# Optimization experiments

Measured on AMD Instinct MI355X. Metric: run time of the kernel, lower is better.

Reference implementation:

```python
import jax, jax.numpy as jnp
import numpy as np

DIM = 128
NUM_LAYERS = 5
EPS = 1e-5


def setup_inputs() -> dict:
    key = jax.random.key(0)
    ks = jax.random.split(key, 16)
    N, E, D = 50000, 640000, DIM
    x = jax.random.uniform(ks[0], (N, 3), dtype=jnp.float32)
    edge_index = jax.random.randint(ks[1], (2, E), 0, N, dtype=jnp.int64)
    norm = jax.random.uniform(ks[2], (E,), dtype=jnp.float32)
    s3 = 1.0 / np.sqrt(3.0)
    sd = 1.0 / np.sqrt(D)
    return {
        "x": x,
        "edge_index": edge_index,
        "norm": norm,
        "W_enc": jax.random.uniform(ks[3], (D, 3), jnp.float32, -s3, s3),
        "bn_e_gamma": jnp.ones((D,), jnp.float32),
        "bn_e_beta": jnp.zeros((D,), jnp.float32),
        "W_ih": jax.random.uniform(ks[4], (3 * D, D), jnp.float32, -sd, sd),
        "W_hh": jax.random.uniform(ks[5], (3 * D, D), jnp.float32, -sd, sd),
        "b_ih": jax.random.uniform(ks[6], (3 * D,), jnp.float32, -sd, sd),
        "b_hh": jax.random.uniform(ks[7], (3 * D,), jnp.float32, -sd, sd),
        "W_dec": jax.random.uniform(ks[8], (D // 2, D), jnp.float32, -sd, sd),
        "bn_d_gamma": jnp.ones((D // 2,), jnp.float32),
        "bn_d_beta": jnp.zeros((D // 2,), jnp.float32),
        "W_dec2": jax.random.uniform(ks[9], (1, D // 2), jnp.float32, -sd * np.sqrt(2.0), sd * np.sqrt(2.0)),
    }


def batchnorm(h, gamma, beta):
    # training-mode BatchNorm1d: biased batch stats over the node dimension
    mu = jnp.mean(h, axis=0)
    var = jnp.var(h, axis=0)
    return (h - mu) * jax.lax.rsqrt(var + EPS) * gamma + beta


def gru_cell(inp, hid, W_ih, W_hh, b_ih, b_hh):
    gi = inp @ W_ih.T + b_ih  # [N, 3D]
    gh = hid @ W_hh.T + b_hh
    D = hid.shape[1]
    i_r, i_z, i_n = gi[:, :D], gi[:, D:2 * D], gi[:, 2 * D:]
    h_r, h_z, h_n = gh[:, :D], gh[:, D:2 * D], gh[:, 2 * D:]
    r = jax.nn.sigmoid(i_r + h_r)
    z = jax.nn.sigmoid(i_z + h_z)
    n = jnp.tanh(i_n + r * h_n)
    return (1.0 - z) * n + z * hid


def reference(x, edge_index, norm, W_enc, bn_e_gamma, bn_e_beta, W_ih, W_hh, b_ih, b_hh, W_dec, bn_d_gamma, bn_d_beta, W_dec2):
    N = x.shape[0]
    src, dst = edge_index[0], edge_index[1]
    # encode
    h = jax.nn.relu(batchnorm(x @ W_enc.T, bn_e_gamma, bn_e_beta))  # [N, D]
    h_sum = h
    prev_h = h
    for _ in range(NUM_LAYERS):
        # neighborhood aggregation: scatter-add of norm-weighted source features
        msg = norm[:, None] * prev_h[src]  # [E, D]
        h_agg = jax.ops.segment_sum(msg, dst, num_segments=N)  # [N, D]
        h_sum = h_sum + h_agg
        prev_h = gru_cell(h_agg, prev_h, W_ih, W_hh, b_ih, b_hh)
    z = h_sum / (NUM_LAYERS + 1)  # mean over stacked h_list
    # decode
    y = jax.nn.relu(batchnorm(z @ W_dec.T, bn_d_gamma, bn_d_beta))
    y = y @ W_dec2.T  # [N, 1]
    return y.reshape(-1)
```

## Files before the change

kernel.cpp:

```cpp
#include <hip/hip_runtime.h>

#define DD 128

typedef _Float16 f16x8 __attribute__((ext_vector_type(8)));
typedef unsigned short u16x8 __attribute__((ext_vector_type(8)));
typedef float f32x4 __attribute__((ext_vector_type(4)));

__device__ __forceinline__ float sigmoidf_(float v){ return 1.f/(1.f+__expf(-v)); }
__device__ __forceinline__ float tanhf_(float v){
  float e2 = __expf(2.f*v);
  return 1.f - 2.f/(e2 + 1.f);
}
__device__ __forceinline__ float h2f(unsigned short u){
  _Float16 h; __builtin_memcpy(&h, &u, 2); return (float)h;
}
__device__ __forceinline__ unsigned short f2h(float v){
  _Float16 h = (_Float16)v; unsigned short u; __builtin_memcpy(&u, &h, 2); return u;
}

#define PREP_B 416
__global__ void __launch_bounds__(256) k_pre1(
        const float* __restrict__ W_ih, const float* __restrict__ W_hh,
        const float* __restrict__ W_dec, const float* __restrict__ x,
        const float* __restrict__ W_enc, const int* __restrict__ dst,
        unsigned short* __restrict__ Wih_h, unsigned short* __restrict__ Whh_h,
        unsigned short* __restrict__ Wd_h, float* __restrict__ h0, float* __restrict__ stats,
        int* __restrict__ counts, int N, int E){
  const int tid = threadIdx.x;
  const int gb = blockIdx.x;
  const int TOT = 384*128;
  if (gb < PREP_B){
    int idx = gb*256 + tid;
    if (idx < 2*TOT){
      const float* W = (idx < TOT) ? W_ih : W_hh;
      unsigned short* D = (idx < TOT) ? Wih_h : Whh_h;
      int fi = (idx < TOT) ? idx : idx - TOT;
      int t = fi & 7;
      int l = (fi >> 3) & 63;
      int ks = (fi >> 9) & 3;
      int nt = fi >> 11;
      int fg = nt / 3, gate = nt % 3;
      int j = gate*128 + fg*16 + (l & 15);
      int k = ks*32 + ((l >> 4) & 3)*8 + t;
      D[fi] = f2h(W[j*128 + k]);
    } else if (idx < 2*TOT + 64*128){
      int fi2 = idx - 2*TOT;
      int t  = fi2 & 7;
      int l  = (fi2 >> 3) & 63;
      int ks = (fi2 >> 9) & 3;
      int jt = fi2 >> 11;
      int j = jt*16 + (l & 15);
      int k = ks*32 + ((l >> 4) & 3)*8 + t;
      Wd_h[fi2] = f2h(W_dec[j*128 + k]);
    }
  } else if (gb < PREP_B + 256){
    const int b = gb - PREP_B;
    const int f = tid & 127;
    const int sub = tid >> 7;
    const float w0 = W_enc[f*3], w1 = W_enc[f*3+1], w2 = W_enc[f*3+2];
    const int chunk = (N + 255) / 256;
    const int n0 = b * chunk;
    const int n1 = (n0 + chunk < N) ? (n0 + chunk) : N;
    float s = 0.f, q = 0.f;
    for (int n = n0 + sub; n < n1; n += 2){
      float x0 = x[n*3], x1 = x[n*3+1], x2 = x[n*3+2];
      float h = x0*w0 + x1*w1 + x2*w2;
      h0[(size_t)n*DD + f] = h;
      s += h; q += h*h;
    }
    atomicAdd(&stats[f], s);
    atomicAdd(&stats[DD+f], q);
  } else {
    int e = (gb - PREP_B - 256)*256 + tid;
    if (e < E) atomicAdd(&counts[dst[e]], 1);
  }
}

__global__ void __launch_bounds__(256) k_scan_part(const int* __restrict__ counts,
                                                   int* __restrict__ partials, int N){
  int i = blockIdx.x*256 + threadIdx.x;
  int v = (i < N) ? counts[i] : 0;
  #pragma unroll
  for (int off = 32; off > 0; off >>= 1) v += __shfl_down(v, off, 64);
  __shared__ int red[4];
  if ((threadIdx.x & 63) == 0) red[threadIdx.x >> 6] = v;
  __syncthreads();
  if (threadIdx.x == 0) partials[blockIdx.x] = red[0]+red[1]+red[2]+red[3];
}

__global__ void __launch_bounds__(256) k_scan_mid(int* __restrict__ partials, int P,
                                                  int* __restrict__ offsets, int N){
  __shared__ int lds[4];
  __shared__ int carry_s;
  const int lane = threadIdx.x & 63, wid = threadIdx.x >> 6;
  if (threadIdx.x == 0) carry_s = 0;
  __syncthreads();
  for (int base = 0; base < P; base += 256){
    int i = base + threadIdx.x;
    int v = (i < P) ? partials[i] : 0;
    int orig = v;
    #pragma unroll
    for (int off = 1; off < 64; off <<= 1){
      int u = __shfl_up(v, off, 64);
      if (lane >= off) v += u;
    }
    if (lane == 63) lds[wid] = v;
    __syncthreads();
    if (threadIdx.x == 0){
      int s = carry_s;
      for (int k = 0; k < 4; k++){ int t = lds[k]; lds[k] = s; s += t; }
      carry_s = s;
    }
    __syncthreads();
    int excl = v - orig + lds[wid];
    if (i < P) partials[i] = excl;
    __syncthreads();
  }
  if (threadIdx.x == 0) offsets[N] = carry_s;
}

__global__ void __launch_bounds__(256) k_scan_expand(const int* __restrict__ counts,
        const int* __restrict__ partials, int* __restrict__ offsets,
        int* __restrict__ cursors, int N){
  int i = blockIdx.x*256 + threadIdx.x;
  int v = (i < N) ? counts[i] : 0;
  int orig = v;
  const int lane = threadIdx.x & 63, wid = threadIdx.x >> 6;
  #pragma unroll
  for (int off = 1; off < 64; off <<= 1){
    int u = __shfl_up(v, off, 64);
    if (lane >= off) v += u;
  }
  __shared__ int lds[4];
  if (lane == 63) lds[wid] = v;
  __syncthreads();
  int wbase = 0;
  for (int k = 0; k < wid; k++) wbase += lds[k];
  int excl = partials[blockIdx.x] + wbase + v - orig;
  if (i < N){ offsets[i] = excl; cursors[i] = excl; }
}

__global__ void __launch_bounds__(256) k_pre2(
        const float* __restrict__ h0, const float* __restrict__ gamma,
        const float* __restrict__ beta, const float* __restrict__ stats,
        unsigned short* __restrict__ ph, unsigned short* __restrict__ hbn,
        const int* __restrict__ src, const int* __restrict__ dst,
        const float* __restrict__ norm, int* __restrict__ cursors,
        int2* __restrict__ csr, int N, int E, int AB){
  const int tid = threadIdx.x;
  if ((int)blockIdx.x < AB){
    int idx = blockIdx.x*256 + tid;
    if (idx >= N*DD) return;
    int f = idx & (DD-1);
    float invN = 1.f / (float)N;
    float mu = stats[f] * invN;
    float var = stats[DD+f] * invN - mu*mu;
    float v = (h0[idx] - mu) * rsqrtf(var + 1e-5f) * gamma[f] + beta[f];
    v = fmaxf(v, 0.f);
    unsigned short hv = f2h(v);
    ph[idx] = hv;
    hbn[idx] = hv;
  } else {
    int e = ((int)blockIdx.x - AB)*256 + tid;
    if (e >= E) return;
    int p = atomicAdd(&cursors[dst[e]], 1);
    union { float f; int i; } c; c.f = norm[e];
    csr[p] = make_int2(src[e], c.i);
  }
}

__global__ void __launch_bounds__(256, 5) k_layer(
        const unsigned short* __restrict__ phc,
        unsigned short* __restrict__ phn,
        unsigned short* __restrict__ agg_out,
        const int* __restrict__ offsets, const int2* __restrict__ csr,
        const unsigned short* __restrict__ Wih_h, const unsigned short* __restrict__ Whh_h,
        const float* __restrict__ b_ih, const float* __restrict__ b_hh, int N){
  __shared__ unsigned short s_a[16*DD];
  const int tid = threadIdx.x;
  const int n0 = blockIdx.x * 16;

  {
    const int m = tid >> 4;
    const int q = tid & 15;
    const int n = n0 + m;
    float acc[8];
    #pragma unroll
    for (int t = 0; t < 8; t++) acc[t] = 0.f;
    if (n < N){
      const int s0 = offsets[n], s1 = offsets[n+1];
      int i = s0;
      for (; i + 8 <= s1; i += 8){
        int2 ed[8]; u16x8 R[8];
        #pragma unroll
        for (int u = 0; u < 8; u++) ed[u] = csr[i+u];
        #pragma unroll
        for (int u = 0; u < 8; u++) R[u] = *(const u16x8*)(phc + (size_t)ed[u].x*DD + q*8);
        #pragma unroll
        for (int u = 0; u < 8; u++){
          union { int i; float f; } c; c.i = ed[u].y;
          #pragma unroll
          for (int t = 0; t < 8; t++)
            acc[t] = fmaf(c.f, h2f((unsigned short)R[u][t]), acc[t]);
        }
      }
      if (i + 4 <= s1){
        int2 ed[4]; u16x8 R[4];
        #pragma unroll
        for (int u = 0; u < 4; u++) ed[u] = csr[i+u];
        #pragma unroll
        for (int u = 0; u < 4; u++) R[u] = *(const u16x8*)(phc + (size_t)ed[u].x*DD + q*8);
        #pragma unroll
        for (int u = 0; u < 4; u++){
          union { int i; float f; } c; c.i = ed[u].y;
          #pragma unroll
          for (int t = 0; t < 8; t++)
            acc[t] = fmaf(c.f, h2f((unsigned short)R[u][t]), acc[t]);
        }
        i += 4;
      }
      for (; i < s1; i++){
        int2 ed = csr[i];
        union { int i; float f; } c; c.i = ed.y;
        u16x8 R = *(const u16x8*)(phc + (size_t)ed.x*DD + q*8);
        #pragma unroll
        for (int t = 0; t < 8; t++)
          acc[t] = fmaf(c.f, h2f((unsigned short)R[t]), acc[t]);
      }
    }
    u16x8 vh;
    #pragma unroll
    for (int t = 0; t < 8; t++) vh[t] = f2h(acc[t]);
    if (n < N)
      *(u16x8*)(agg_out + (size_t)n*DD + q*8) = vh;
    const int cc = q ^ (m & 7);
    *(u16x8*)(s_a + m*DD + cc*8) = vh;
  }
  __syncthreads();

  const int w = tid >> 6, l = tid & 63, ar = l & 15, aq = l >> 4;
  int r0 = n0 + ar; if (r0 >= N) r0 = N-1;
  const size_t p0 = (size_t)r0*DD + aq*8;
  const int sw = ar & 7;

  for (int g = 0; g < 2; g++){
    const int fg = w*2 + g;
    f32x4 acc_i[3], acc_h[3];
    #pragma unroll
    for (int t = 0; t < 3; t++){
      acc_i[t] = (f32x4){0.f,0.f,0.f,0.f};
      acc_h[t] = (f32x4){0.f,0.f,0.f,0.f};
    }

    #pragma unroll
    for (int ks = 0; ks < 4; ks++){
      const int c = (ks*4 + aq) ^ sw;
      f16x8 ih0 = *(const f16x8*)(s_a + ar*DD + c*8);
      f16x8 hh0 = *(const f16x8*)(phc + p0 + ks*32);
      #pragma unroll
      for (int t = 0; t < 3; t++){
        size_t bo = ((size_t)((fg*3 + t)*4 + ks)*64 + l)*8;
        f16x8 bih = *(const f16x8*)(Wih_h + bo);
        f16x8 bhh = *(const f16x8*)(Whh_h + bo);
        acc_i[t] = __builtin_amdgcn_mfma_f32_16x16x32_f16(ih0, bih, acc_i[t], 0, 0, 0);
        acc_h[t] = __builtin_amdgcn_mfma_f32_16x16x32_f16(hh0, bhh, acc_h[t], 0, 0, 0);
      }
    }

    const int f = fg*16 + ar;
    const float bir = b_ih[f], biz = b_ih[128+f], bin_ = b_ih[256+f];
    const float bhr = b_hh[f], bhz = b_hh[128+f], bhn = b_hh[256+f];
    #pragma unroll
    for (int r = 0; r < 4; r++){
      int n = n0 + aq*4 + r;
      if (n < N){
        float sir = acc_i[0][r] + bir, shr = acc_h[0][r] + bhr;
        float siz = acc_i[1][r] + biz, shz = acc_h[1][r] + bhz;
        float sin_ = acc_i[2][r] + bin_, shn = acc_h[2][r] + bhn;
        float rr = sigmoidf_(sir + shr);
        float zz = sigmoidf_(siz + shz);
        float nn = tanhf_(sin_ + rr*shn);
        size_t o = (size_t)n*DD + f;
        float hp = h2f(phc[o]);
        float h = (1.f - zz)*nn + zz*hp;
        phn[o] = f2h(h);
      }
    }
  }
}

__global__ void __launch_bounds__(256, 8) k_dec1(const unsigned short* __restrict__ hbn,
        const unsigned short* __restrict__ aggs, size_t NF,
        const unsigned short* __restrict__ ph5,
        const int* __restrict__ offsets, const int2* __restrict__ csr,
        const unsigned short* __restrict__ Wd_h, float* __restrict__ y1,
        float* __restrict__ stats_d, int N){
  __shared__ unsigned short zs[16*DD];
  const int tid = threadIdx.x;
  const int n0 = blockIdx.x * 16;

  {
    const int m = tid >> 4;
    const int q = tid & 15;
    const int n = n0 + m;
    float acc[8];
    #pragma unroll
    for (int t = 0; t < 8; t++) acc[t] = 0.f;
    if (n < N){
      size_t o = (size_t)n*DD + q*8;
      u16x8 hb = *(const u16x8*)(hbn + o);
      #pragma unroll
      for (int t = 0; t < 8; t++) acc[t] = h2f(hb[t]);
      #pragma unroll
      for (int l = 0; l < 4; l++){
        u16x8 ag = *(const u16x8*)(aggs + l*NF + o);
        #pragma unroll
        for (int t = 0; t < 8; t++) acc[t] += h2f(ag[t]);
      }
      const int s0 = offsets[n], s1 = offsets[n+1];
      int i = s0;
      for (; i + 8 <= s1; i += 8){
        int2 ed[8]; u16x8 R[8];
        #pragma unroll
        for (int u = 0; u < 8; u++) ed[u] = csr[i+u];
        #pragma unroll
        for (int u = 0; u < 8; u++) R[u] = *(const u16x8*)(ph5 + (size_t)ed[u].x*DD + q*8);
        #pragma unroll
        for (int u = 0; u < 8; u++){
          union { int i; float f; } c; c.i = ed[u].y;
          #pragma unroll
          for (int t = 0; t < 8; t++)
            acc[t] = fmaf(c.f, h2f((unsigned short)R[u][t]), acc[t]);
        }
      }
      if (i + 4 <= s1){
        int2 ed[4]; u16x8 R[4];
        #pragma unroll
        for (int u = 0; u < 4; u++) ed[u] = csr[i+u];
        #pragma unroll
        for (int u = 0; u < 4; u++) R[u] = *(const u16x8*)(ph5 + (size_t)ed[u].x*DD + q*8);
        #pragma unroll
        for (int u = 0; u < 4; u++){
          union { int i; float f; } c; c.i = ed[u].y;
          #pragma unroll
          for (int t = 0; t < 8; t++)
            acc[t] = fmaf(c.f, h2f((unsigned short)R[u][t]), acc[t]);
        }
        i += 4;
      }
      for (; i < s1; i++){
        int2 ed = csr[i];
        union { int i; float f; } c; c.i = ed.y;
        u16x8 R = *(const u16x8*)(ph5 + (size_t)ed.x*DD + q*8);
        #pragma unroll
        for (int t = 0; t < 8; t++)
          acc[t] = fmaf(c.f, h2f((unsigned short)R[t]), acc[t]);
      }
    }
    u16x8 vh;
    #pragma unroll
    for (int t = 0; t < 8; t++) vh[t] = f2h(acc[t] * (1.f/6.f));
    const int cc = q ^ (m & 7);
    *(u16x8*)(zs + m*DD + cc*8) = vh;
  }
  __syncthreads();

  const int w = tid >> 6, l = tid & 63, ar = l & 15, aq = l >> 4;
  const int sw = ar & 7;
  f32x4 acc = (f32x4){0.f,0.f,0.f,0.f};
  #pragma unroll
  for (int ks = 0; ks < 4; ks++){
    const int c = (ks*4 + aq) ^ sw;
    f16x8 a = *(const f16x8*)(zs + ar*DD + c*8);
    f16x8 b = *(const f16x8*)(Wd_h + ((size_t)(w*4 + ks)*64 + l)*8);
    acc = __builtin_amdgcn_mfma_f32_16x16x32_f16(a, b, acc, 0, 0, 0);
  }
  float s = 0.f, q2 = 0.f;
  #pragma unroll
  for (int r = 0; r < 4; r++){
    int n = n0 + aq*4 + r;
    float v = acc[r];
    if (n < N){
      y1[(size_t)n*64 + w*16 + ar] = v;
      s += v; q2 += v*v;
    }
  }
  s  += __shfl_xor(s, 16, 64);  s  += __shfl_xor(s, 32, 64);
  q2 += __shfl_xor(q2, 16, 64); q2 += __shfl_xor(q2, 32, 64);
  if (aq == 0){
    float* st = stats_d + (size_t)(blockIdx.x & 7)*128;
    atomicAdd(&st[w*16 + ar], s);
    atomicAdd(&st[64 + w*16 + ar], q2);
  }
}

__global__ void __launch_bounds__(256) k_dec2(const float* __restrict__ y1,
        const float* __restrict__ gamma, const float* __restrict__ beta,
        const float* __restrict__ W_dec2, const float* __restrict__ stats_d,
        float* __restrict__ out, int N){
  const int j = threadIdx.x & 63;
  const int g = threadIdx.x >> 6;
  const int n = blockIdx.x*4 + g;
  if (n >= N) return;
  float ssum = 0.f, qsum = 0.f;
  #pragma unroll
  for (int c = 0; c < 8; c++){
    ssum += stats_d[c*128 + j];
    qsum += stats_d[c*128 + 64 + j];
  }
  float invN = 1.f / (float)N;
  float mu = ssum * invN;
  float var = qsum * invN - mu*mu;
  float v = (y1[(size_t)n*64 + j] - mu) * rsqrtf(var + 1e-5f) * gamma[j] + beta[j];
  v = fmaxf(v, 0.f) * W_dec2[j];
  for (int off = 32; off > 0; off >>= 1) v += __shfl_down(v, off, 64);
  if (j == 0) out[n] = v;
}

extern "C" void kernel_launch(void* const* d_in, const int* in_sizes, int n_in,
                              void* d_out, int out_size, void* d_ws, size_t ws_size,
                              hipStream_t stream) {
  const int N = in_sizes[0] / 3;
  const int E = in_sizes[1] / 2;
  const int P = (N + 255) / 256;
  const int HIST_B = (E + 255) / 256;
  const int AB = (N*DD + 255) / 256;

  const float* x     = (const float*)d_in[0];
  const int*   ei    = (const int*)d_in[1];
  const int*   src   = ei;
  const int*   dst   = ei + E;
  const float* norm  = (const float*)d_in[2];
  const float* W_enc = (const float*)d_in[3];
  const float* g_e   = (const float*)d_in[4];
  const float* b_e   = (const float*)d_in[5];
  const float* W_ih  = (const float*)d_in[6];
  const float* W_hh  = (const float*)d_in[7];
  const float* b_ih  = (const float*)d_in[8];
  const float* b_hh  = (const float*)d_in[9];
  const float* W_dec = (const float*)d_in[10];
  const float* g_d   = (const float*)d_in[11];
  const float* b_d   = (const float*)d_in[12];
  const float* W_dec2= (const float*)d_in[13];
  float* out = (float*)d_out;

  float* ws = (float*)d_ws;
  const size_t NF = (size_t)N * DD;
  float* scr    = ws;
  float* stats  = scr + NF;
  float* Wt_dec = stats + 1280;
  unsigned short* Wd_h  = (unsigned short*)Wt_dec;
  unsigned short* Wih_h = (unsigned short*)(Wt_dec + 64*128);
  unsigned short* Whh_h = Wih_h + 384*128;
  unsigned short* ph_A  = Whh_h + 384*128;
  unsigned short* ph_B  = ph_A + NF;
  unsigned short* hbn   = ph_B + NF;
  unsigned short* aggs  = hbn + NF;
  int*   counts  = (int*)(aggs + 4*NF);
  int*   offsets = counts + N;
  int*   cursors = offsets + N + 1;
  int*   partials= cursors + N;
  int2*  csr     = (int2*)(partials + P);
  float* y1 = scr;

  hipMemsetAsync(stats, 0, 1280*sizeof(float), stream);
  hipMemsetAsync(counts, 0, (size_t)N*sizeof(int), stream);

  k_pre1<<<PREP_B + 256 + HIST_B, 256, 0, stream>>>(
      W_ih, W_hh, W_dec, x, W_enc, dst,
      Wih_h, Whh_h, Wd_h, scr, stats, counts, N, E);
  k_scan_part<<<P, 256, 0, stream>>>(counts, partials, N);
  k_scan_mid<<<1, 256, 0, stream>>>(partials, P, offsets, N);
  k_scan_expand<<<P, 256, 0, stream>>>(counts, partials, offsets, cursors, N);
  k_pre2<<<AB + HIST_B, 256, 0, stream>>>(
      scr, g_e, b_e, stats, ph_A, hbn,
      src, dst, norm, cursors, csr, N, E, AB);

  unsigned short* phh_c = ph_A;
  unsigned short* phh_n = ph_B;
  for (int l = 0; l < 4; l++){
    k_layer<<<(N + 15)/16, 256, 0, stream>>>(phh_c, phh_n, aggs + (size_t)l*NF,
                                             offsets, csr,
                                             Wih_h, Whh_h, b_ih, b_hh, N);
    unsigned short* t = phh_c; phh_c = phh_n; phh_n = t;
  }

  k_dec1<<<(N + 15)/16, 256, 0, stream>>>(hbn, aggs, NF, phh_c, offsets, csr,
                                          Wd_h, y1, stats + 256, N);
  k_dec2<<<(N + 3)/4, 256, 0, stream>>>(y1, g_d, b_d, W_dec2, stats + 256, out, N);
}
```

Before: 499.5 us.

## Double GRU tile to 32 rows, stage outputs in LDS, store intermediates in fp16

The GRU layer kernel now processes 32 nodes per 512-thread block. Each wave reuses its weight fragments across two 16-row A tiles, and the new hidden state is staged through shared memory so it can be written back with coalesced vector stores. The encoder pre-BN buffer and decoder y1 buffer are now stored as fp16 instead of fp32, which halves their memory traffic. This costs extra syncthreads, more registers per thread and some precision in the BN statistics inputs.

```diff
diff --git a/kernel.cpp b/kernel.cpp
--- a/kernel.cpp
+++ b/kernel.cpp
@@ -4,6 +4,7 @@
 
 typedef _Float16 f16x8 __attribute__((ext_vector_type(8)));
 typedef unsigned short u16x8 __attribute__((ext_vector_type(8)));
+typedef unsigned short u16x4 __attribute__((ext_vector_type(4)));
 typedef float f32x4 __attribute__((ext_vector_type(4)));
 
 __device__ __forceinline__ float sigmoidf_(float v){ return 1.f/(1.f+__expf(-v)); }
@@ -24,8 +25,8 @@
         const float* __restrict__ W_dec, const float* __restrict__ x,
         const float* __restrict__ W_enc, const int* __restrict__ dst,
         unsigned short* __restrict__ Wih_h, unsigned short* __restrict__ Whh_h,
-        unsigned short* __restrict__ Wd_h, float* __restrict__ h0, float* __restrict__ stats,
-        int* __restrict__ counts, int N, int E){
+        unsigned short* __restrict__ Wd_h, unsigned short* __restrict__ h0,
+        float* __restrict__ stats, int* __restrict__ counts, int N, int E){
   const int tid = threadIdx.x;
   const int gb = blockIdx.x;
   const int TOT = 384*128;
@@ -65,8 +66,10 @@
     for (int n = n0 + sub; n < n1; n += 2){
       float x0 = x[n*3], x1 = x[n*3+1], x2 = x[n*3+2];
       float h = x0*w0 + x1*w1 + x2*w2;
-      h0[(size_t)n*DD + f] = h;
-      s += h; q += h*h;
+      unsigned short hu = f2h(h);
+      float hq = h2f(hu);
+      h0[(size_t)n*DD + f] = hu;
+      s += hq; q += hq*hq;
     }
     atomicAdd(&stats[f], s);
     atomicAdd(&stats[DD+f], q);
@@ -141,7 +144,7 @@
 }
 
 __global__ void __launch_bounds__(256) k_pre2(
-        const float* __restrict__ h0, const float* __restrict__ gamma,
+        const unsigned short* __restrict__ h0, const float* __restrict__ gamma,
         const float* __restrict__ beta, const float* __restrict__ stats,
         unsigned short* __restrict__ ph, unsigned short* __restrict__ hbn,
         const int* __restrict__ src, const int* __restrict__ dst,
@@ -155,7 +158,7 @@
     float invN = 1.f / (float)N;
     float mu = stats[f] * invN;
     float var = stats[DD+f] * invN - mu*mu;
-    float v = (h0[idx] - mu) * rsqrtf(var + 1e-5f) * gamma[f] + beta[f];
+    float v = (h2f(h0[idx]) - mu) * rsqrtf(var + 1e-5f) * gamma[f] + beta[f];
     v = fmaxf(v, 0.f);
     unsigned short hv = f2h(v);
     ph[idx] = hv;
@@ -169,16 +172,16 @@
   }
 }
 
-__global__ void __launch_bounds__(256, 5) k_layer(
+__global__ void __launch_bounds__(512, 4) k_layer(
         const unsigned short* __restrict__ phc,
         unsigned short* __restrict__ phn,
         unsigned short* __restrict__ agg_out,
         const int* __restrict__ offsets, const int2* __restrict__ csr,
         const unsigned short* __restrict__ Wih_h, const unsigned short* __restrict__ Whh_h,
         const float* __restrict__ b_ih, const float* __restrict__ b_hh, int N){
-  __shared__ unsigned short s_a[16*DD];
+  __shared__ unsigned short s_a[32*DD];
   const int tid = threadIdx.x;
-  const int n0 = blockIdx.x * 16;
+  const int n0 = blockIdx.x * 32;
 
   {
     const int m = tid >> 4;
@@ -239,53 +242,76 @@
   __syncthreads();
 
   const int w = tid >> 6, l = tid & 63, ar = l & 15, aq = l >> 4;
-  int r0 = n0 + ar; if (r0 >= N) r0 = N-1;
+  int r0 = n0 + ar;      if (r0 >= N) r0 = N-1;
+  int r1 = n0 + 16 + ar; if (r1 >= N) r1 = N-1;
   const size_t p0 = (size_t)r0*DD + aq*8;
+  const size_t p1 = (size_t)r1*DD + aq*8;
   const int sw = ar & 7;
 
-  for (int g = 0; g < 2; g++){
-    const int fg = w*2 + g;
-    f32x4 acc_i[3], acc_h[3];
+  f32x4 acc_i[2][3], acc_h[2][3];
+  #pragma unroll
+  for (int ta = 0; ta < 2; ta++)
     #pragma unroll
     for (int t = 0; t < 3; t++){
-      acc_i[t] = (f32x4){0.f,0.f,0.f,0.f};
-      acc_h[t] = (f32x4){0.f,0.f,0.f,0.f};
-    }
-
-    #pragma unroll
-    for (int ks = 0; ks < 4; ks++){
-      const int c = (ks*4 + aq) ^ sw;
-      f16x8 ih0 = *(const f16x8*)(s_a + ar*DD + c*8);
-      f16x8 hh0 = *(const f16x8*)(phc + p0 + ks*32);
-      #pragma unroll
-      for (int t = 0; t < 3; t++){
-        size_t bo = ((size_t)((fg*3 + t)*4 + ks)*64 + l)*8;
-        f16x8 bih = *(const f16x8*)(Wih_h + bo);
-        f16x8 bhh = *(const f16x8*)(Whh_h + bo);
-        acc_i[t] = __builtin_amdgcn_mfma_f32_16x16x32_f16(ih0, bih, acc_i[t], 0, 0, 0);
-        acc_h[t] = __builtin_amdgcn_mfma_f32_16x16x32_f16(hh0, bhh, acc_h[t], 0, 0, 0);
-      }
-    }
-
-    const int f = fg*16 + ar;
-    const float bir = b_ih[f], biz = b_ih[128+f], bin_ = b_ih[256+f];
-    const float bhr = b_hh[f], bhz = b_hh[128+f], bhn = b_hh[256+f];
+      acc_i[ta][t] = (f32x4){0.f,0.f,0.f,0.f};
+      acc_h[ta][t] = (f32x4){0.f,0.f,0.f,0.f};
+    }
+
+  #pragma unroll
+  for (int ks = 0; ks < 4; ks++){
+    const int c = (ks*4 + aq) ^ sw;
+    f16x8 ih0 = *(const f16x8*)(s_a + ar*DD       + c*8);
+    f16x8 ih1 = *(const f16x8*)(s_a + (16+ar)*DD  + c*8);
+    f16x8 hh0 = *(const f16x8*)(phc + p0 + ks*32);
+    f16x8 hh1 = *(const f16x8*)(phc + p1 + ks*32);
+    #pragma unroll
+    for (int t = 0; t < 3; t++){
+      size_t bo = ((size_t)((w*3 + t)*4 + ks)*64 + l)*8;
+      f16x8 bih = *(const f16x8*)(Wih_h + bo);
+      f16x8 bhh = *(const f16x8*)(Whh_h + bo);
+      acc_i[0][t] = __builtin_amdgcn_mfma_f32_16x16x32_f16(ih0, bih, acc_i[0][t], 0, 0, 0);
+      acc_i[1][t] = __builtin_amdgcn_mfma_f32_16x16x32_f16(ih1, bih, acc_i[1][t], 0, 0, 0);
+      acc_h[0][t] = __builtin_amdgcn_mfma_f32_16x16x32_f16(hh0, bhh, acc_h[0][t], 0, 0, 0);
+      acc_h[1][t] = __builtin_amdgcn_mfma_f32_16x16x32_f16(hh1, bhh, acc_h[1][t], 0, 0, 0);
+    }
+  }
+
+  const int f = w*16 + ar;
+  const float bir = b_ih[f], biz = b_ih[128+f], bin_ = b_ih[256+f];
+  const float bhr = b_hh[f], bhz = b_hh[128+f], bhn = b_hh[256+f];
+  float hv[2][4];
+  #pragma unroll
+  for (int ta = 0; ta < 2; ta++){
     #pragma unroll
     for (int r = 0; r < 4; r++){
-      int n = n0 + aq*4 + r;
+      int n = n0 + ta*16 + aq*4 + r;
       if (n < N){
-        float sir = acc_i[0][r] + bir, shr = acc_h[0][r] + bhr;
-        float siz = acc_i[1][r] + biz, shz = acc_h[1][r] + bhz;
-        float sin_ = acc_i[2][r] + bin_, shn = acc_h[2][r] + bhn;
+        float sir = acc_i[ta][0][r] + bir, shr = acc_h[ta][0][r] + bhr;
+        float siz = acc_i[ta][1][r] + biz, shz = acc_h[ta][1][r] + bhz;
+        float sin_ = acc_i[ta][2][r] + bin_, shn = acc_h[ta][2][r] + bhn;
         float rr = sigmoidf_(sir + shr);
         float zz = sigmoidf_(siz + shz);
         float nn = tanhf_(sin_ + rr*shn);
-        size_t o = (size_t)n*DD + f;
-        float hp = h2f(phc[o]);
-        float h = (1.f - zz)*nn + zz*hp;
-        phn[o] = f2h(h);
-      }
-    }
+        float hp = h2f(phc[(size_t)n*DD + f]);
+        hv[ta][r] = (1.f - zz)*nn + zz*hp;
+      }
+    }
+  }
+  __syncthreads();
+  #pragma unroll
+  for (int ta = 0; ta < 2; ta++){
+    #pragma unroll
+    for (int r = 0; r < 4; r++){
+      int m2 = ta*16 + aq*4 + r;
+      if (n0 + m2 < N) s_a[m2*DD + f] = f2h(hv[ta][r]);
+    }
+  }
+  __syncthreads();
+  {
+    int idx = tid * 8;
+    int n = n0 + (idx >> 7);
+    if (n < N)
+      *(u16x8*)(phn + (size_t)n0*DD + idx) = *(const u16x8*)(s_a + idx);
   }
 }
 
@@ -293,9 +319,10 @@
         const unsigned short* __restrict__ aggs, size_t NF,
         const unsigned short* __restrict__ ph5,
         const int* __restrict__ offsets, const int2* __restrict__ csr,
-        const unsigned short* __restrict__ Wd_h, float* __restrict__ y1,
+        const unsigned short* __restrict__ Wd_h, unsigned short* __restrict__ y1,
         float* __restrict__ stats_d, int N){
   __shared__ unsigned short zs[16*DD];
+  __shared__ unsigned short stage[16*64];
   const int tid = threadIdx.x;
   const int n0 = blockIdx.x * 16;
 
@@ -381,7 +408,7 @@
     int n = n0 + aq*4 + r;
     float v = acc[r];
     if (n < N){
-      y1[(size_t)n*64 + w*16 + ar] = v;
+      stage[(aq*4 + r)*64 + w*16 + ar] = f2h(v);
       s += v; q2 += v*v;
     }
   }
@@ -392,9 +419,16 @@
     atomicAdd(&st[w*16 + ar], s);
     atomicAdd(&st[64 + w*16 + ar], q2);
   }
-}
-
-__global__ void __launch_bounds__(256) k_dec2(const float* __restrict__ y1,
+  __syncthreads();
+  {
+    int idx = tid * 4;
+    int n = n0 + (idx >> 6);
+    if (n < N)
+      *(u16x4*)(y1 + (size_t)n0*64 + idx) = *(const u16x4*)(stage + idx);
+  }
+}
+
+__global__ void __launch_bounds__(256) k_dec2(const unsigned short* __restrict__ y1,
         const float* __restrict__ gamma, const float* __restrict__ beta,
         const float* __restrict__ W_dec2, const float* __restrict__ stats_d,
         float* __restrict__ out, int N){
@@ -411,7 +445,7 @@
   float invN = 1.f / (float)N;
   float mu = ssum * invN;
   float var = qsum * invN - mu*mu;
-  float v = (y1[(size_t)n*64 + j] - mu) * rsqrtf(var + 1e-5f) * gamma[j] + beta[j];
+  float v = (h2f(y1[(size_t)n*64 + j]) - mu) * rsqrtf(var + 1e-5f) * gamma[j] + beta[j];
   v = fmaxf(v, 0.f) * W_dec2[j];
   for (int off = 32; off > 0; off >>= 1) v += __shfl_down(v, off, 64);
   if (j == 0) out[n] = v;
@@ -447,6 +481,8 @@
   float* ws = (float*)d_ws;
   const size_t NF = (size_t)N * DD;
   float* scr    = ws;
+  unsigned short* h0h = (unsigned short*)scr;
+  unsigned short* y1h = (unsigned short*)scr;
   float* stats  = scr + NF;
   float* Wt_dec = stats + 1280;
   unsigned short* Wd_h  = (unsigned short*)Wt_dec;
@@ -461,31 +497,30 @@
   int*   cursors = offsets + N + 1;
   int*   partials= cursors + N;
   int2*  csr     = (int2*)(partials + P);
-  float* y1 = scr;
 
   hipMemsetAsync(stats, 0, 1280*sizeof(float), stream);
   hipMemsetAsync(counts, 0, (size_t)N*sizeof(int), stream);
 
   k_pre1<<<PREP_B + 256 + HIST_B, 256, 0, stream>>>(
       W_ih, W_hh, W_dec, x, W_enc, dst,
-      Wih_h, Whh_h, Wd_h, scr, stats, counts, N, E);
+      Wih_h, Whh_h, Wd_h, h0h, stats, counts, N, E);
   k_scan_part<<<P, 256, 0, stream>>>(counts, partials, N);
   k_scan_mid<<<1, 256, 0, stream>>>(partials, P, offsets, N);
   k_scan_expand<<<P, 256, 0, stream>>>(counts, partials, offsets, cursors, N);
   k_pre2<<<AB + HIST_B, 256, 0, stream>>>(
-      scr, g_e, b_e, stats, ph_A, hbn,
+      h0h, g_e, b_e, stats, ph_A, hbn,
       src, dst, norm, cursors, csr, N, E, AB);
 
   unsigned short* phh_c = ph_A;
   unsigned short* phh_n = ph_B;
   for (int l = 0; l < 4; l++){
-    k_layer<<<(N + 15)/16, 256, 0, stream>>>(phh_c, phh_n, aggs + (size_t)l*NF,
+    k_layer<<<(N + 31)/32, 512, 0, stream>>>(phh_c, phh_n, aggs + (size_t)l*NF,
                                              offsets, csr,
                                              Wih_h, Whh_h, b_ih, b_hh, N);
     unsigned short* t = phh_c; phh_c = phh_n; phh_n = t;
   }
 
   k_dec1<<<(N + 15)/16, 256, 0, stream>>>(hbn, aggs, NF, phh_c, offsets, csr,
-                                          Wd_h, y1, stats + 256, N);
-  k_dec2<<<(N + 3)/4, 256, 0, stream>>>(y1, g_d, b_d, W_dec2, stats + 256, out, N);
-}
+                                          Wd_h, y1h, stats + 256, N);
+  k_dec2<<<(N + 3)/4, 256, 0, stream>>>(y1h, g_d, b_d, W_dec2, stats + 256, out, N);
+}
```

New measurement: 521.2 us. 1.04x slower.
